# Optimization experiments

Measured on AMD Instinct MI355X. Metric: run time of the kernel, lower is better.

Reference implementation:

```python
import jax, jax.numpy as jnp
import numpy as np

GRID = 32            # sqrt(num_embeddings=1024)
COMMIT = 0.25        # commitment_cost
TOPO_W = 0.35        # topo_weight
EPS = 1e-12          # torch F.normalize eps


def _l2norm(x):
    return x / jnp.maximum(jnp.linalg.norm(x, axis=-1, keepdims=True), EPS)


def setup_inputs() -> dict:
    key = jax.random.key(0)
    k1, k2 = jax.random.split(key)
    z_e = jax.random.normal(k1, (32, 256, 64, 64), dtype=jnp.float32)
    # embedding.weight ~ N(0, (1/num_embeddings)^2), shape [num_embeddings, embedding_dim]
    weight = jax.random.normal(k2, (GRID * GRID, 256), dtype=jnp.float32) * (1.0 / (GRID * GRID))
    return {"z_e": z_e, "weight": weight}


def reference(z_e, weight):
    B, C, H, W = z_e.shape
    z = jnp.transpose(z_e, (0, 2, 3, 1))            # BHWC
    flat = _l2norm(z.reshape(-1, C))                # [N, C], N = B*H*W
    norm_w = _l2norm(weight)                        # [K, C]
    # cosine distance argmin (no_grad in torch; indices are int so no grad anyway)
    distances = 2.0 - 2.0 * (flat @ norm_w.T)       # [N, K]
    idx = jnp.argmin(distances, axis=1)             # [N]
    z_q = norm_w[idx].reshape(B, H, W, C)
    z_e_norm = flat.reshape(B, H, W, C)
    loss_commit = jnp.mean((jax.lax.stop_gradient(z_q) - z_e_norm) ** 2)
    loss_dict = jnp.mean((z_q - jax.lax.stop_gradient(z_e_norm)) ** 2)
    vq_loss = loss_dict + COMMIT * loss_commit
    # topology grid smoothness loss (with wraparound terms)
    gw = norm_w.reshape(GRID, GRID, C)
    loss_topo = (jnp.mean((gw[:, 1:, :] - gw[:, :-1, :]) ** 2)
                 + jnp.mean((gw[1:, :, :] - gw[:-1, :, :]) ** 2)
                 + jnp.mean((gw[:, 0, :] - gw[:, -1, :]) ** 2)
                 + jnp.mean((gw[0, :, :] - gw[-1, :, :]) ** 2)) * TOPO_W
    # straight-through estimator
    z_q_ste = z_e_norm + jax.lax.stop_gradient(z_q - z_e_norm)
    z_q_out = jnp.transpose(z_q_ste, (0, 3, 1, 2))  # back to BCHW
    return (z_q_out, vq_loss, idx.reshape(B, H, W), loss_topo)
```

## Files before the change

kernel.cpp:

```cpp
#include <hip/hip_runtime.h>
#include <cstdint>
#include <cstddef>

#define C_ 256
#define HW_ 4096
#define N_ 131072
#define K_ 1024
#define VQ_OFF   33554432
#define IDX_OFF  33554433
#define TOPO_OFF 33685505
#define VQ_SCALE (1.25f / 33554432.0f)
#define REFINE_TAU 4e-3f
#define MARK 2048

typedef _Float16 half8  __attribute__((ext_vector_type(8)));
typedef float    f32x16 __attribute__((ext_vector_type(16)));
typedef float    f32x4  __attribute__((ext_vector_type(4)));


__device__ __forceinline__ float mul_nofuse(float a, float b) {
    float t = a * b;
    asm volatile("" : "+v"(t));
    return t;
}

__device__ __forceinline__ float np_sumsq128(const float* x) {
    float r[8];
    #pragma unroll
    for (int j = 0; j < 8; j++) r[j] = mul_nofuse(x[j], x[j]);
    for (int i = 8; i < 128; i += 8) {
        #pragma unroll
        for (int j = 0; j < 8; j++) r[j] += mul_nofuse(x[i + j], x[i + j]);
    }
    return ((r[0] + r[1]) + (r[2] + r[3])) + ((r[4] + r[5]) + (r[6] + r[7]));
}

__device__ __forceinline__ float np_norm256(const float* x) {
    float ss = np_sumsq128(x) + np_sumsq128(x + 128);
    return sqrtf(ss);
}

__device__ __forceinline__ void stage16(const half8* g, half8* l) {
    __builtin_amdgcn_global_load_lds(
        (const __attribute__((address_space(1))) void*)g,
        (__attribute__((address_space(3))) void*)l, 16, 0, 0);
}

__global__ __launch_bounds__(256)
void k_normw(const float* __restrict__ w, float* __restrict__ wT,
             float* __restrict__ wN, half8* __restrict__ cbH,
             half8* __restrict__ cbL, float* __restrict__ out) {
    __shared__ float lw[64][257];
    __shared__ float nrm_sh[64];
    int tid = threadIdx.x;
    if (blockIdx.x == 0 && tid == 0) {
        out[VQ_OFF] = 0.0f;
        out[TOPO_OFF] = 0.0f;
    }
    int r0 = blockIdx.x << 6;
    #pragma unroll
    for (int it = 0; it < 64; it++) {
        int f = (it << 8) + tid;
        int row = f >> 8, c = f & 255;
        lw[row][c] = w[((size_t)(r0 + row) << 8) + c];
    }
    __syncthreads();
    if (tid < 64) nrm_sh[tid] = fmaxf(np_norm256(&lw[tid][0]), 1e-12f);
    __syncthreads();
    int rr = tid & 63, cg = tid >> 6;
    float nr = nrm_sh[rr];
    for (int c = cg; c < C_; c += 4) {
        wT[(c << 10) + r0 + rr] = lw[rr][c] / nr;
    }
    int cw = r0 + rr;
    int cwblk = cw >> 5, lrow = cw & 31;
    #pragma unroll
    for (int o8 = cg; o8 < 32; o8 += 4) {
        int c0 = o8 << 3;
        half8 H, L;
        float vv[8];
        #pragma unroll
        for (int i = 0; i < 8; i++) {
            float v = lw[rr][c0 + i] / nr;
            vv[i] = v;
            _Float16 hh = (_Float16)v;
            H[i] = hh;
            L[i] = (_Float16)(v - (float)hh);
        }
        float4* wnp = reinterpret_cast<float4*>(wN + ((size_t)cw << 8) + c0);
        wnp[0] = make_float4(vv[0], vv[1], vv[2], vv[3]);
        wnp[1] = make_float4(vv[4], vv[5], vv[6], vv[7]);
        int fidx = ((cwblk << 4) + (o8 >> 1)) * 64 + lrow + ((o8 & 1) << 5);
        cbH[fidx] = H;
        cbL[fidx] = L;
    }
}

__global__ void k_topo(const float* __restrict__ wT, float* __restrict__ out) {
    const float W12 = 0.35f / (32.0f * 31.0f * 256.0f);
    const float W34 = 0.35f / (32.0f * 256.0f);
    float acc = 0.0f;
    int base = (blockIdx.x << 8) + threadIdx.x;
    #pragma unroll
    for (int i = 0; i < 4; i++) {
        int e = base + (i << 16);
        int k = e & 1023;
        int ii = k >> 5, jj = k & 31;
        float v = wT[e];
        if (jj < 31)  { float d = wT[e + 1]   - v; acc += d * d * W12; }
        if (ii < 31)  { float d = wT[e + 32]  - v; acc += d * d * W12; }
        if (jj == 31) { float d = wT[e - 31]  - v; acc += d * d * W34; }
        if (ii == 31) { float d = wT[e - 992] - v; acc += d * d * W34; }
    }
    for (int off = 32; off > 0; off >>= 1) acc += __shfl_xor(acc, off);
    __shared__ float red[4];
    if ((threadIdx.x & 63) == 0) red[threadIdx.x >> 6] = acc;
    __syncthreads();
    if (threadIdx.x == 0) atomicAdd(out + TOPO_OFF, red[0] + red[1] + red[2] + red[3]);
}

__device__ __forceinline__ float max16(const f32x16& a) {
    float m0 = fmaxf(fmaxf(a[0], a[1]),  fmaxf(a[2], a[3]));
    float m1 = fmaxf(fmaxf(a[4], a[5]),  fmaxf(a[6], a[7]));
    float m2 = fmaxf(fmaxf(a[8], a[9]),  fmaxf(a[10], a[11]));
    float m3 = fmaxf(fmaxf(a[12], a[13]), fmaxf(a[14], a[15]));
    return fmaxf(fmaxf(m0, m1), fmaxf(m2, m3));
}

__device__ __forceinline__ void fold_tile(const f32x16& a, int W, int g,
                                          float& bv, float& sv, int& bi) {
    float M = max16(a);
    if (M >= bv) {
        #pragma unroll
        for (int r = 0; r < 16; r++) {
            float v = a[r];
            int k = (W << 5) + (r & 3) + ((r >> 2) << 3) + (g << 2);
            if (v > bv) { sv = bv; bv = v; bi = k; }
            else sv = fmaxf(sv, v);
        }
    } else {
        sv = fmaxf(sv, M);
    }
}

__global__ __launch_bounds__(256, 2)
void k_main(const float* __restrict__ z, const float* __restrict__ wN,
            const half8* __restrict__ cbH, const half8* __restrict__ cbL,
            float* __restrict__ out) {
    __shared__ half8 sbuf[2][1024];

    int tid  = threadIdx.x;
    int lane = tid & 63, wv = tid >> 6;
    int g    = lane >> 5, l31 = lane & 31;
    int blk  = blockIdx.x;
    int b    = blk >> 5;
    int wpx  = ((blk & 31) << 7) + (wv << 5);
    const float* zb = z + ((size_t)b << 20);

    #pragma unroll
    for (int i = 0; i < 4; i++) {
        int u = (wv << 2) + i;
        stage16(cbH + (u << 6) + lane, &sbuf[0][u << 6]);
    }

    half8 Bf[16];
    float np0 = 0.0f;
    #pragma unroll
    for (int ks = 0; ks < 16; ks++) {
        const float* zp = zb + ((size_t)((ks << 4) + (g << 3)) << 12) + wpx + l31;
        half8 h;
        float s = 0.0f;
        #pragma unroll
        for (int i = 0; i < 8; i++) {
            float v = zp[(size_t)i << 12];
            s += v * v;
            h[i] = (_Float16)v;
        }
        np0 += s;
        Bf[ks] = h;
    }
    __syncthreads();

    float bv0 = -3e38f, sv0 = -3e38f;
    int bi0 = 0;
    #pragma unroll 1
    for (int W = 0; W < 32; W++) {
        f32x16 acc = {};
        #pragma unroll
        for (int pl = 0; pl < 2; pl++) {
            if (!(W == 31 && pl == 1)) {
                const half8* src = pl ? (cbH + ((W + 1) << 10)) : (cbL + (W << 10));
                #pragma unroll
                for (int i = 0; i < 4; i++) {
                    int u = (wv << 2) + i;
                    stage16(src + (u << 6) + lane, &sbuf[pl ^ 1][u << 6]);
                }
            }
            #pragma unroll
            for (int ks = 0; ks < 16; ks++) {
                half8 A = sbuf[pl][(ks << 6) + lane];
                acc = __builtin_amdgcn_mfma_f32_32x32x16_f16(A, Bf[ks], acc, 0, 0, 0);
            }
            __syncthreads();
        }
        fold_tile(acc, W, g, bv0, sv0, bi0);
    }

    float BV0, SV0; int BI0;
    {
        float obv = __shfl_xor(bv0, 32), osv = __shfl_xor(sv0, 32);
        int obi = __shfl_xor(bi0, 32);
        if (obv > bv0 || (obv == bv0 && obi < bi0)) { BV0 = obv; BI0 = obi; SV0 = fmaxf(osv, bv0); }
        else                                        { BV0 = bv0; BI0 = bi0; SV0 = fmaxf(sv0, obv); }
    }
    float nn0 = np0 + __shfl_xor(np0, 32);

    float dsum = 0.0f;
    if (lane < 32) {
        int fi = BI0;
        if (BV0 - SV0 < REFINE_TAU) fi += MARK;
        out[IDX_OFF + (b << 12) + wpx + lane] = (float)fi;
        float rinv = 1.0f / fmaxf(sqrtf(nn0), 1e-12f);
        dsum = 2.0f - 2.0f * BV0 * rinv;
    }
    #pragma unroll
    for (int off = 32; off > 0; off >>= 1) dsum += __shfl_xor(dsum, off);
    if (lane == 0) atomicAdd(out + VQ_OFF, dsum * VQ_SCALE);

    const float4* wrow = reinterpret_cast<const float4*>(wN + ((size_t)BI0 << 8) + ((size_t)g << 7));
    size_t ob = ((size_t)b << 20) + ((size_t)g << 19) + (size_t)(wpx + l31);
    #pragma unroll 4
    for (int c4 = 0; c4 < 32; c4++) {
        float4 q = wrow[c4];
        out[ob + ((size_t)((c4 << 2) + 0) << 12)] = q.x;
        out[ob + ((size_t)((c4 << 2) + 1) << 12)] = q.y;
        out[ob + ((size_t)((c4 << 2) + 2) << 12)] = q.z;
        out[ob + ((size_t)((c4 << 2) + 3) << 12)] = q.w;
    }
}

template<int P>
__device__ __forceinline__ void refine_chunk(
    int b, const int* q, const int* koldq, int done, int act,
    const float* __restrict__ z, const float* __restrict__ wT,
    float* __restrict__ out,
    float (*flz)[256], float (*rrs)[16], float* nn,
    float (*wredd)[4], int (*wredk)[4], int* knew_sh) {
    int tid = threadIdx.x;

    #pragma unroll
    for (int p = 0; p < P; p++) {
        float v = 0.0f;
        if (p < act) {
            int hw = q[done + p] & 4095;
            v = z[((size_t)((b << 8) + tid) << 12) + hw];
        }
        flz[p][tid] = v;
    }
    __syncthreads();

    if (tid < 16 * P) {
        int p = tid >> 4, w = tid & 15;
        const float* x = &flz[p][0];
        int base = ((w >> 3) << 7) + (w & 7);
        float r = mul_nofuse(x[base], x[base]);
        #pragma unroll
        for (int i = 1; i < 16; i++) {
            float xv = x[base + (i << 3)];
            r += mul_nofuse(xv, xv);
        }
        rrs[p][w] = r;
    }
    __syncthreads();
    if (tid < P) {
        const float* rp = rrs[tid];
        float s0 = ((rp[0] + rp[1]) + (rp[2] + rp[3])) + ((rp[4] + rp[5]) + (rp[6] + rp[7]));
        float s1 = ((rp[8] + rp[9]) + (rp[10] + rp[11])) + ((rp[12] + rp[13]) + (rp[14] + rp[15]));
        nn[tid] = fmaxf(sqrtf(s0 + s1), 1e-12f);
    }
    __syncthreads();
    #pragma unroll
    for (int p = 0; p < P; p++) flz[p][tid] = flz[p][tid] / nn[p];
    __syncthreads();

    float a0[P], a1[P], a2[P], a3[P];
    #pragma unroll
    for (int p = 0; p < P; p++) { a0[p] = 0.f; a1[p] = 0.f; a2[p] = 0.f; a3[p] = 0.f; }
    #pragma unroll 1
    for (int c0 = 0; c0 < C_; c0 += 4) {
        f32x4 fz[P];
        #pragma unroll
        for (int p = 0; p < P; p++)
            fz[p] = *reinterpret_cast<const f32x4*>(&flz[p][c0]);
        #pragma unroll
        for (int j = 0; j < 4; j++) {
            const float* col = wT + ((c0 + j) << 10) + tid;
            float w0 = col[0], w1 = col[256], w2 = col[512], w3 = col[768];
            #pragma unroll
            for (int p = 0; p < P; p++) {
                float a = fz[p][j];
                a0[p] = fmaf(a, w0, a0[p]);
                a1[p] = fmaf(a, w1, a1[p]);
                a2[p] = fmaf(a, w2, a2[p]);
                a3[p] = fmaf(a, w3, a3[p]);
            }
        }
    }

    int lane = tid & 63, wv = tid >> 6;
    #pragma unroll
    for (int p = 0; p < P; p++) {
        float dbest = 1e30f; int kbest = 0;
        { float d = 2.0f - 2.0f * a0[p]; if (d < dbest) { dbest = d; kbest = tid;       } }
        { float d = 2.0f - 2.0f * a1[p]; if (d < dbest) { dbest = d; kbest = tid + 256; } }
        { float d = 2.0f - 2.0f * a2[p]; if (d < dbest) { dbest = d; kbest = tid + 512; } }
        { float d = 2.0f - 2.0f * a3[p]; if (d < dbest) { dbest = d; kbest = tid + 768; } }
        #pragma unroll
        for (int off = 32; off > 0; off >>= 1) {
            float d2 = __shfl_xor(dbest, off);
            int   k2 = __shfl_xor(kbest, off);
            if (d2 < dbest || (d2 == dbest && k2 < kbest)) { dbest = d2; kbest = k2; }
        }
        if (lane == 0) { wredd[p][wv] = dbest; wredk[p][wv] = kbest; }
    }
    __syncthreads();
    if (tid < P) {
        float dbest = wredd[tid][0]; int kbest = wredk[tid][0];
        #pragma unroll
        for (int w = 1; w < 4; w++) {
            float d2 = wredd[tid][w]; int k2 = wredk[tid][w];
            if (d2 < dbest || (d2 == dbest && k2 < kbest)) { dbest = d2; kbest = k2; }
        }
        knew_sh[tid] = kbest;
    }
    __syncthreads();

    for (int p = 0; p < act; p++) {
        int n    = q[done + p];
        int kold = koldq[done + p];
        int knew = knew_sh[p];
        if (tid == 0) out[IDX_OFF + n] = (float)knew;
        if (knew != kold) {
            int hw = n & 4095;
            out[((size_t)((b << 8) + tid) << 12) + hw] = wT[(tid << 10) + knew];
            if (tid == 0) {
                float ao = 0.f, an = 0.f;
                for (int c = 0; c < C_; c++) {
                    ao = fmaf(flz[p][c], wT[(c << 10) + kold], ao);
                    an = fmaf(flz[p][c], wT[(c << 10) + knew], an);
                }
                atomicAdd(out + VQ_OFF, ((2.0f - 2.0f * an) - (2.0f - 2.0f * ao)) * VQ_SCALE);
            }
        }
    }
}

__global__ __launch_bounds__(256)
void k_refine(const float* __restrict__ z, const float* __restrict__ wT,
              float* __restrict__ out) {
    __shared__ float flz[8][256];
    __shared__ float rrs[8][16];
    __shared__ float nn[8];
    __shared__ float wredd[8][4];
    __shared__ int   wredk[8][4];
    __shared__ int   knew_sh[8];
    __shared__ int   q[256];
    __shared__ int   koldq[256];
    __shared__ int   wcnt[4];
    int tid  = threadIdx.x;
    int base = blockIdx.x << 8;
    int b    = base >> 12;

    float fidx = out[IDX_OFF + base + tid];
    bool marked = fidx >= (float)MARK;
    unsigned long long mask = __ballot(marked);
    int lane = tid & 63, wv = tid >> 6;
    if (lane == 0) wcnt[wv] = __popcll(mask);
    __syncthreads();
    int off = 0;
    for (int w = 0; w < wv; w++) off += wcnt[w];
    if (marked) {
        int slot = off + __popcll(mask & ((1ull << lane) - 1ull));
        q[slot] = base + tid;
        koldq[slot] = (int)fidx - MARK;
    }
    __syncthreads();
    int cnt = wcnt[0] + wcnt[1] + wcnt[2] + wcnt[3];
    if (cnt == 0) return;

    int done = 0;
    while (done < cnt) {
        int rem = cnt - done;
        int act;
        if (rem >= 5) {
            act = rem > 8 ? 8 : rem;
            refine_chunk<8>(b, q, koldq, done, act, z, wT, out, flz, rrs, nn, wredd, wredk, knew_sh);
        } else if (rem >= 3) {
            act = rem;
            refine_chunk<4>(b, q, koldq, done, act, z, wT, out, flz, rrs, nn, wredd, wredk, knew_sh);
        } else if (rem == 2) {
            act = 2;
            refine_chunk<2>(b, q, koldq, done, act, z, wT, out, flz, rrs, nn, wredd, wredk, knew_sh);
        } else {
            act = 1;
            refine_chunk<1>(b, q, koldq, done, act, z, wT, out, flz, rrs, nn, wredd, wredk, knew_sh);
        }
        done += act;
        __syncthreads();
    }
}

extern "C" void kernel_launch(void* const* d_in, const int* in_sizes, int n_in,
                              void* d_out, int out_size, void* d_ws, size_t ws_size,
                              hipStream_t stream) {
    const float* z = (const float*)d_in[0];
    const float* w = (const float*)d_in[1];
    float* out = (float*)d_out;
    float* wT  = (float*)d_ws;
    float* wN  = wT + 262144;
    half8* cbH = (half8*)(wT + 524288);
    half8* cbL = (half8*)(wT + 655360);

    hipLaunchKernelGGL(k_normw,  dim3(16),   dim3(256), 0, stream, w, wT, wN, cbH, cbL, out);
    hipLaunchKernelGGL(k_topo,   dim3(256),  dim3(256), 0, stream, wT, out);
    hipLaunchKernelGGL(k_main,   dim3(1024), dim3(256), 0, stream, z, wN, cbH, cbL, out);
    hipLaunchKernelGGL(k_refine, dim3(512),  dim3(256), 0, stream, z, wT, out);
}
```

Before: 464.9 us.

## Triple-buffer codebook staging in half-size chunks with explicit vmcnt waits

```diff
diff --git a/kernel.cpp b/kernel.cpp
--- a/kernel.cpp
+++ b/kernel.cpp
@@ -147,7 +147,7 @@
 void k_main(const float* __restrict__ z, const float* __restrict__ wN,
             const half8* __restrict__ cbH, const half8* __restrict__ cbL,
             float* __restrict__ out) {
-    __shared__ half8 sbuf[2][1024];
+    __shared__ half8 sbuf[3][512];
 
     int tid  = threadIdx.x;
     int lane = tid & 63, wv = tid >> 6;
@@ -158,9 +158,10 @@
     const float* zb = z + ((size_t)b << 20);
 
     #pragma unroll
-    for (int i = 0; i < 4; i++) {
-        int u = (wv << 2) + i;
+    for (int i = 0; i < 2; i++) {
+        int u = (wv << 1) + i;
         stage16(cbH + (u << 6) + lane, &sbuf[0][u << 6]);
+        stage16(cbH + ((u + 8) << 6) + lane, &sbuf[1][u << 6]);
     }
 
     half8 Bf[16];
@@ -183,27 +184,39 @@
 
     float bv0 = -3e38f, sv0 = -3e38f;
     int bi0 = 0;
+    f32x16 acc = {};
     #pragma unroll 1
-    for (int W = 0; W < 32; W++) {
-        f32x16 acc = {};
-        #pragma unroll
-        for (int pl = 0; pl < 2; pl++) {
-            if (!(W == 31 && pl == 1)) {
-                const half8* src = pl ? (cbH + ((W + 1) << 10)) : (cbL + (W << 10));
-                #pragma unroll
-                for (int i = 0; i < 4; i++) {
-                    int u = (wv << 2) + i;
-                    stage16(src + (u << 6) + lane, &sbuf[pl ^ 1][u << 6]);
-                }
+    for (int G = 0; G < 128; G++) {
+        int slot = G % 3;
+        if (G + 2 < 128) {
+            int nG = G + 2;
+            const half8* src = ((nG >> 1) & 1) ? (cbL + ((nG >> 2) << 10))
+                                               : (cbH + ((nG >> 2) << 10));
+            src += (nG & 1) << 9;
+            int ns = nG % 3;
+            #pragma unroll
+            for (int i = 0; i < 2; i++) {
+                int u = (wv << 1) + i;
+                stage16(src + (u << 6) + lane, &sbuf[ns][u << 6]);
             }
+        }
+        int ksb = (G & 1) << 3;
+        #pragma unroll
+        for (int k8 = 0; k8 < 8; k8++) {
+            half8 A = sbuf[slot][(k8 << 6) + lane];
+            acc = __builtin_amdgcn_mfma_f32_32x32x16_f16(A, Bf[ksb + k8], acc, 0, 0, 0);
+        }
+        if ((G & 3) == 3) {
+            fold_tile(acc, G >> 2, g, bv0, sv0, bi0);
             #pragma unroll
-            for (int ks = 0; ks < 16; ks++) {
-                half8 A = sbuf[pl][(ks << 6) + lane];
-                acc = __builtin_amdgcn_mfma_f32_32x32x16_f16(A, Bf[ks], acc, 0, 0, 0);
-            }
-            __syncthreads();
-        }
-        fold_tile(acc, W, g, bv0, sv0, bi0);
+            for (int r = 0; r < 16; r++) acc[r] = 0.0f;
+        }
+        if (G + 2 < 128)      { asm volatile("s_waitcnt vmcnt(2)" ::: "memory"); }
+        else if (G + 1 < 128) { asm volatile("s_waitcnt vmcnt(0)" ::: "memory"); }
+        if (G + 1 < 128) {
+            __builtin_amdgcn_s_barrier();
+            __builtin_amdgcn_sched_barrier(0);
+        }
     }
 
     float BV0, SV0; int BI0;
```

Result: slower. 914.1 us (+96.6%).
